# Performance work log

Hardware: AMD Instinct MI355X
Metric: run time of the kernel (lower is better)

## Reference

```python
import jax, jax.numpy as jnp
import numpy as np

EPS = 1e-3  # denominator regularizer for weighted mean/cov
DIST_SCALE = 10.0  # raw_call applies 10.0 * distsq before exp weighting

V, K, C, F = 100000, 40, 3, 32


def setup_inputs() -> dict:
    key = jax.random.key(0)
    k1, k2, k3, k4 = jax.random.split(key, 4)
    coordinates = jax.random.normal(k1, (V, C), dtype=jnp.float32)
    distsq = jax.random.uniform(k2, (V, K), dtype=jnp.float32)  # squared distances >= 0
    features = jax.random.uniform(k3, (V, F), dtype=jnp.float32)  # non-negative activations
    n_idxs = jax.random.randint(k4, (V, K), 0, V, dtype=jnp.int32)
    return {"coordinates": coordinates, "distsq": distsq, "features": features, "n_idxs": n_idxs}


def reference(coordinates, distsq, features, n_idxs):
    nV, nC = coordinates.shape
    nF = features.shape[1]
    # SelectWithDefault semantics: index -1 -> default 0
    valid = (n_idxs >= 0)
    idx = jnp.where(valid, n_idxs, 0)
    n_coords = jnp.where(valid[..., None], coordinates[idx], 0.0)  # V x K x C
    w = jnp.exp(-DIST_SCALE * distsq)  # V x K distance weights
    n_feat = jnp.where(valid[..., None], features[idx], 0.0) * w[..., None]  # V x K x F (feature weights)
    wsum = jnp.sum(n_feat, axis=1)  # V x F
    denom = wsum[:, :, None] + EPS  # V x F x 1
    # weighted first moment -> means, weighted second moment -> covariance
    means = jnp.einsum('vkf,vkc->vfc', n_feat, n_coords) / denom  # V x F x C
    second = jnp.einsum('vkf,vkc,vkd->vfcd', n_feat, n_coords, n_coords) / denom[..., None]  # V x F x C x C
    cov = second - means[:, :, :, None] * means[:, :, None, :]  # centered covariance
    out = jnp.concatenate([cov.reshape(nV, nF * nC * nC), means.reshape(nV, nF * nC)], axis=-1)
    return out
```

## Files before the change

### kernel.cpp

```cpp
#include <hip/hip_runtime.h>


constexpr int K = 40;
constexpr int C = 3;
constexpr int F = 32;
constexpr float EPS = 1e-3f;
constexpr float DIST_SCALE = 10.0f;
constexpr int OUT_PER_V = F * C * C + F * C;
constexpr int VPB = 8;
constexpr int PAIRS = VPB * K;
constexpr int OUT_DW = VPB * OUT_PER_V;
constexpr int OUT_F4 = OUT_DW / 4;

typedef float floatx4 __attribute__((ext_vector_type(4)));
typedef float v2f     __attribute__((ext_vector_type(2)));

__global__ __launch_bounds__(256) void neighcov_kernel(
    const float* __restrict__ coords,
    const float* __restrict__ distsq,
    const float* __restrict__ features,
    const int*   __restrict__ nidx,
    float* __restrict__ out,
    int V)
{
    __shared__ float4  s_a[PAIRS];
    __shared__ float4  s_b[PAIRS];
    __shared__ v2f     s_c[PAIRS];
    __shared__ int     s_joff[PAIRS];
    __shared__ floatx4 s_out4[OUT_F4];

    const int tid   = threadIdx.x;
    const int vbase = blockIdx.x * VPB;
    const long long total_pairs = (long long)V * K;

    #pragma unroll
    for (int p = tid; p < PAIRS; p += 256) {
        const long long gp = (long long)vbase * K + p;
        int idx = -1;
        float d = 0.f;
        if (gp < total_pairs) {
            idx = __builtin_nontemporal_load(nidx + gp);
            d   = __builtin_nontemporal_load(distsq + gp);
        }
        const bool valid = (idx >= 0);
        const int j = valid ? idx : 0;
        const float w = valid ? __expf(-DIST_SCALE * d) : 0.f;
        const float x = coords[(size_t)j * 3 + 0];
        const float y = coords[(size_t)j * 3 + 1];
        const float z = coords[(size_t)j * 3 + 2];
        const float wx = w * x, wy = w * y, wz = w * z;
        s_a[p] = make_float4(w, wx, wy, wz);
        s_b[p] = make_float4(wx * x, wx * y, wx * z, wy * y);
        s_c[p] = (v2f){wy * z, wz * z};
        s_joff[p] = j * F;
    }
    __syncthreads();

    const int f    = tid & (F - 1);
    const int vloc = tid >> 5;

    const v2f* a2 = (const v2f*)(s_a + vloc * K);
    const v2f* b2 = (const v2f*)(s_b + vloc * K);
    const v2f* c2 = s_c + vloc * K;
    const int* jp = s_joff + vloc * K;

    v2f acc0 = {0.f, 0.f};
    v2f acc1 = {0.f, 0.f};
    v2f acc2 = {0.f, 0.f};
    v2f acc3 = {0.f, 0.f};
    v2f acc4 = {0.f, 0.f};

    #pragma unroll 8
    for (int k = 0; k < K; ++k) {
        const v2f a_lo = a2[2 * k];
        const v2f a_hi = a2[2 * k + 1];
        const v2f b_lo = b2[2 * k];
        const v2f b_hi = b2[2 * k + 1];
        const v2f cc   = c2[k];
        const int jo   = jp[k];
        const float feat = features[jo + f];
        const v2f fv = {feat, feat};
        acc0 = __builtin_elementwise_fma(a_lo, fv, acc0);
        acc1 = __builtin_elementwise_fma(a_hi, fv, acc1);
        acc2 = __builtin_elementwise_fma(b_lo, fv, acc2);
        acc3 = __builtin_elementwise_fma(b_hi, fv, acc3);
        acc4 = __builtin_elementwise_fma(cc,   fv, acc4);
    }

    const float wsum = acc0.x, m0 = acc0.y, m1 = acc1.x, m2 = acc1.y;
    const float s00 = acc2.x, s01 = acc2.y, s02 = acc3.x;
    const float s11 = acc3.y, s12 = acc4.x, s22 = acc4.y;

    const float inv = 1.f / (wsum + EPS);
    const float mu0 = m0 * inv, mu1 = m1 * inv, mu2 = m2 * inv;
    const float c00 = s00 * inv - mu0 * mu0;
    const float c01 = s01 * inv - mu0 * mu1;
    const float c02 = s02 * inv - mu0 * mu2;
    const float c11 = s11 * inv - mu1 * mu1;
    const float c12 = s12 * inv - mu1 * mu2;
    const float c22 = s22 * inv - mu2 * mu2;

    float* s_out = (float*)s_out4;
    float* so = s_out + vloc * OUT_PER_V + f * 9;
    so[0] = c00; so[1] = c01; so[2] = c02;
    so[3] = c01; so[4] = c11; so[5] = c12;
    so[6] = c02; so[7] = c12; so[8] = c22;
    float* sm = s_out + vloc * OUT_PER_V + F * 9 + f * 3;
    sm[0] = mu0; sm[1] = mu1; sm[2] = mu2;

    __syncthreads();

    const int rem_v  = V - vbase;
    const int lim_f4 = (rem_v >= VPB) ? OUT_F4 : rem_v * (OUT_PER_V / 4);
    floatx4* o4 = (floatx4*)(out + (size_t)vbase * OUT_PER_V);
    #pragma unroll
    for (int g = tid; g < OUT_F4; g += 256) {
        if (g < lim_f4) {
            __builtin_nontemporal_store(s_out4[g], o4 + g);
        }
    }
}

extern "C" void kernel_launch(void* const* d_in, const int* in_sizes, int n_in,
                              void* d_out, int out_size, void* d_ws, size_t ws_size,
                              hipStream_t stream) {
    const float* coords   = (const float*)d_in[0];
    const float* distsq   = (const float*)d_in[1];
    const float* features = (const float*)d_in[2];
    const int*   nidx     = (const int*)d_in[3];
    float* out = (float*)d_out;

    const int V = in_sizes[0] / C;
    const int blocks = (V + VPB - 1) / VPB;

    neighcov_kernel<<<blocks, 256, 0, stream>>>(coords, distsq, features, nidx, out, V);
}
```

Measured before the change: 247.4 us.

## Stage gathered neighbor feature rows into LDS via async global_load_lds

Each wave now loads its 80 neighbor indices into registers, broadcasts row offsets with shuffles, and issues async global-to-LDS loads of full 128-byte feature rows. The main accumulation loop then reads features from shared memory instead of doing per-iteration gathers from global memory. The feature staging buffer is aliased with the output staging area, which needs an extra barrier before the output is written. LDS use grows to about 53 KB per block, which may lower occupancy.

Result: slower. 265.2 us (+7.2%).

```diff
diff --git a/kernel.cpp b/kernel.cpp
--- a/kernel.cpp
+++ b/kernel.cpp
@@ -11,6 +11,14 @@
 constexpr int PAIRS = VPB * K;
 constexpr int OUT_DW = VPB * OUT_PER_V;
 constexpr int OUT_F4 = OUT_DW / 4;
+constexpr int PPW = PAIRS / 4;
+constexpr int ROW_BYTES = F * 4;
+
+constexpr int OFF_A    = 0;
+constexpr int OFF_B    = 5120;
+constexpr int OFF_C    = 10240;
+constexpr int OFF_FEAT = 12800;
+constexpr int SMEM_BYTES = 53760;
 
 typedef float floatx4 __attribute__((ext_vector_type(4)));
 typedef float v2f     __attribute__((ext_vector_type(2)));
@@ -23,46 +31,90 @@
     float* __restrict__ out,
     int V)
 {
-    __shared__ float4  s_a[PAIRS];
-    __shared__ float4  s_b[PAIRS];
-    __shared__ v2f     s_c[PAIRS];
-    __shared__ int     s_joff[PAIRS];
-    __shared__ floatx4 s_out4[OUT_F4];
+    __shared__ __align__(16) char smem[SMEM_BYTES];
+    float4*  s_a    = (float4*)(smem + OFF_A);
+    float4*  s_b    = (float4*)(smem + OFF_B);
+    v2f*     s_c    = (v2f*)(smem + OFF_C);
+    float*   s_feat = (float*)(smem + OFF_FEAT);
+    floatx4* s_out4 = (floatx4*)(smem + OFF_FEAT);
 
     const int tid   = threadIdx.x;
+    const int lane  = tid & 63;
+    const int wv    = tid >> 6;
     const int vbase = blockIdx.x * VPB;
     const long long total_pairs = (long long)V * K;
+    const int pbase = wv * PPW;
 
-    #pragma unroll
-    for (int p = tid; p < PAIRS; p += 256) {
+    int joff1 = 0, joff2 = 0;
+    float w1 = 0.f, w2 = 0.f;
+    {
+        const int p = pbase + lane;
         const long long gp = (long long)vbase * K + p;
-        int idx = -1;
-        float d = 0.f;
+        int idx = -1; float d = 0.f;
         if (gp < total_pairs) {
             idx = __builtin_nontemporal_load(nidx + gp);
             d   = __builtin_nontemporal_load(distsq + gp);
         }
         const bool valid = (idx >= 0);
-        const int j = valid ? idx : 0;
-        const float w = valid ? __expf(-DIST_SCALE * d) : 0.f;
-        const float x = coords[(size_t)j * 3 + 0];
-        const float y = coords[(size_t)j * 3 + 1];
-        const float z = coords[(size_t)j * 3 + 2];
+        joff1 = (valid ? idx : 0) * F;
+        w1 = valid ? __expf(-DIST_SCALE * d) : 0.f;
+    }
+    {
+        int idx = -1; float d = 0.f;
+        if (lane < 16) {
+            const long long gp = (long long)vbase * K + pbase + 64 + lane;
+            if (gp < total_pairs) {
+                idx = __builtin_nontemporal_load(nidx + gp);
+                d   = __builtin_nontemporal_load(distsq + gp);
+            }
+        }
+        const bool valid = (idx >= 0);
+        joff2 = (valid ? idx : 0) * F;
+        w2 = valid ? __expf(-DIST_SCALE * d) : 0.f;
+    }
+
+    #pragma unroll
+    for (int c = 0; c < 10; ++c) {
+        const int sel = 8 * c + (lane >> 3);
+        const int joff = (c < 8) ? __shfl(joff1, sel, 64)
+                                 : __shfl(joff2, sel - 64, 64);
+        const float* gsrc = features + joff + (lane & 7) * 4;
+        char* ldst = smem + OFF_FEAT + (size_t)(pbase + 8 * c) * ROW_BYTES;
+        __builtin_amdgcn_global_load_lds(
+            (const __attribute__((address_space(1))) void*)(const void*)gsrc,
+            (__attribute__((address_space(3))) void*)(void*)ldst,
+            16, 0, 0);
+    }
+
+    {
+        const int p = pbase + lane;
+        const int j3 = (joff1 >> 5) * 3;
+        const float x = coords[j3 + 0], y = coords[j3 + 1], z = coords[j3 + 2];
+        const float w = w1;
         const float wx = w * x, wy = w * y, wz = w * z;
         s_a[p] = make_float4(w, wx, wy, wz);
         s_b[p] = make_float4(wx * x, wx * y, wx * z, wy * y);
         s_c[p] = (v2f){wy * z, wz * z};
-        s_joff[p] = j * F;
     }
+    if (lane < 16) {
+        const int p = pbase + 64 + lane;
+        const int j3 = (joff2 >> 5) * 3;
+        const float x = coords[j3 + 0], y = coords[j3 + 1], z = coords[j3 + 2];
+        const float w = w2;
+        const float wx = w * x, wy = w * y, wz = w * z;
+        s_a[p] = make_float4(w, wx, wy, wz);
+        s_b[p] = make_float4(wx * x, wx * y, wx * z, wy * y);
+        s_c[p] = (v2f){wy * z, wz * z};
+    }
+
     __syncthreads();
 
     const int f    = tid & (F - 1);
     const int vloc = tid >> 5;
-
-    const v2f* a2 = (const v2f*)(s_a + vloc * K);
-    const v2f* b2 = (const v2f*)(s_b + vloc * K);
-    const v2f* c2 = s_c + vloc * K;
-    const int* jp = s_joff + vloc * K;
+    const float4* pa = s_a + vloc * K;
+    const float4* pb = s_b + vloc * K;
+    const v2f*    pc = s_c + vloc * K;
+    const float*  pf = s_feat + (size_t)vloc * K * F + f;
 
     v2f acc0 = {0.f, 0.f};
     v2f acc1 = {0.f, 0.f};
@@ -72,19 +124,16 @@
 
     #pragma unroll 8
     for (int k = 0; k < K; ++k) {
-        const v2f a_lo = a2[2 * k];
-        const v2f a_hi = a2[2 * k + 1];
-        const v2f b_lo = b2[2 * k];
-        const v2f b_hi = b2[2 * k + 1];
-        const v2f cc   = c2[k];
-        const int jo   = jp[k];
-        const float feat = features[jo + f];
+        const float4 a  = pa[k];
+        const float4 b  = pb[k];
+        const v2f    cc = pc[k];
+        const float feat = pf[k * F];
         const v2f fv = {feat, feat};
-        acc0 = __builtin_elementwise_fma(a_lo, fv, acc0);
-        acc1 = __builtin_elementwise_fma(a_hi, fv, acc1);
-        acc2 = __builtin_elementwise_fma(b_lo, fv, acc2);
-        acc3 = __builtin_elementwise_fma(b_hi, fv, acc3);
-        acc4 = __builtin_elementwise_fma(cc,   fv, acc4);
+        acc0 = __builtin_elementwise_fma((v2f){a.x, a.y}, fv, acc0);
+        acc1 = __builtin_elementwise_fma((v2f){a.z, a.w}, fv, acc1);
+        acc2 = __builtin_elementwise_fma((v2f){b.x, b.y}, fv, acc2);
+        acc3 = __builtin_elementwise_fma((v2f){b.z, b.w}, fv, acc3);
+        acc4 = __builtin_elementwise_fma(cc, fv, acc4);
     }
 
     const float wsum = acc0.x, m0 = acc0.y, m1 = acc1.x, m2 = acc1.y;
@@ -100,7 +149,9 @@
     const float c12 = s12 * inv - mu1 * mu2;
     const float c22 = s22 * inv - mu2 * mu2;
 
-    float* s_out = (float*)s_out4;
+    __syncthreads();
+
+    float* s_out = (float*)(smem + OFF_FEAT);
     float* so = s_out + vloc * OUT_PER_V + f * 9;
     so[0] = c00; so[1] = c01; so[2] = c02;
     so[3] = c01; so[4] = c11; so[5] = c12;
```
